# Performance work log

Hardware: AMD Instinct MI355X
Metric: run time of the kernel (lower is better)

Reference implementation:

```python
import jax, jax.numpy as jnp
import numpy as np

G, B, S, D = 4, 1, 1024, 2048   # num_gpus (chunks), batch, seq_local, model dim
H, DH = 32, 64                  # heads, dim_head; inner_dim = H*DH = D
EPS = 1e-6
NEG = -1e30                     # finite stand-in for -inf lse init (grad-safe)


def setup_inputs() -> dict:
    key = jax.random.key(0)
    ks = jax.random.split(key, 8)
    wsc = 1.0 / np.sqrt(D)  # keep pre-softmax logits in a sane range
    return {
        'x':  jax.random.normal(ks[0], (G, B, S, D), jnp.float32),
        'Wq': jax.random.normal(ks[1], (D, D), jnp.float32) * wsc,
        'bq': jnp.zeros((D,), jnp.float32),
        'Wk': jax.random.normal(ks[2], (D, D), jnp.float32) * wsc,
        'bk': jnp.zeros((D,), jnp.float32),
        'Wv': jax.random.normal(ks[3], (D, D), jnp.float32) * wsc,
        'bv': jnp.zeros((D,), jnp.float32),
        'qn_w': jnp.ones((D,), jnp.float32),
        'kn_w': jnp.ones((D,), jnp.float32),
        'Wo': jax.random.normal(ks[4], (D, D), jnp.float32) * wsc,
        'bo': jnp.zeros((D,), jnp.float32),
    }


def _rms_norm(t, w):
    return t * jax.lax.rsqrt(jnp.mean(t * t, axis=-1, keepdims=True) + EPS) * w


def reference(x, Wq, bq, Wk, bk, Wv, bv, qn_w, kn_w, Wo, bo):
    # x: [G, B, S, D] -- per-'GPU' sequence chunks
    q = _rms_norm(x @ Wq.T + bq, qn_w)
    k = _rms_norm(x @ Wk.T + bk, kn_w)
    v = x @ Wv.T + bv
    split = lambda t: t.reshape(G, B, S, H, DH).transpose(0, 1, 3, 2, 4)  # [G,B,H,S,DH]
    q, k, v = split(q), split(k), split(v)
    scale = 1.0 / np.sqrt(DH)

    out = jnp.zeros_like(q)
    lse = jnp.full((G, B, H, S, 1), NEG, q.dtype)
    kc, vc = k, v
    # Ring: each chunk attends to the visiting K/V chunk with online softmax.
    for _ in range(G):
        scores = jnp.einsum('gbhqd,gbhkd->gbhqk', q, kc) * scale
        m = scores.max(axis=-1, keepdims=True)
        e = jnp.exp(scores - m)
        ssum = e.sum(axis=-1, keepdims=True)
        chunk_lse = m + jnp.log(ssum)
        chunk_out = jnp.einsum('gbhqk,gbhkd->gbhqd', e / ssum, vc)
        new_lse = jnp.logaddexp(lse, chunk_lse)
        out = out * jnp.exp(lse - new_lse) + chunk_out * jnp.exp(chunk_lse - new_lse)
        lse = new_lse
        # rotate K/V around the ring: device i receives from device i-1
        kc = jnp.roll(kc, 1, axis=0)
        vc = jnp.roll(vc, 1, axis=0)

    o = out.transpose(0, 1, 3, 2, 4).reshape(G, B, S, H * DH)
    return o @ Wo.T + bo
```

## Files before the change

### kernel.cpp

```cpp
#include <hip/hip_runtime.h>

typedef __bf16 bf16x8 __attribute__((ext_vector_type(8)));
typedef float f32x4 __attribute__((ext_vector_type(4)));
typedef float f32x16 __attribute__((ext_vector_type(16)));
typedef unsigned short u16x8 __attribute__((ext_vector_type(8)));
typedef unsigned u32x2 __attribute__((ext_vector_type(2)));
typedef unsigned u32x4 __attribute__((ext_vector_type(4)));

__device__ __forceinline__ unsigned short f2bf(float f) {
  union { float f; unsigned u; } v; v.f = f;
  unsigned r = (v.u + 0x7fffu + ((v.u >> 16) & 1u)) >> 16;
  return (unsigned short)r;
}
__device__ __forceinline__ float bf2f(unsigned short s) {
  union { unsigned u; float f; } v; v.u = ((unsigned)s) << 16;
  return v.f;
}

#define GLD16(g, l)                                                        \
  __builtin_amdgcn_global_load_lds(                                        \
      (const __attribute__((address_space(1))) void*)(g),                  \
      (__attribute__((address_space(3))) void*)(l), 16, 0, 0)

__device__ __forceinline__ int swzc(int row, int colel) {
  return colel ^ ((((row & 7) ^ ((row >> 3) & 7)) & 7) << 3);
}

__device__ __forceinline__ u32x2 plswap(unsigned a, unsigned b) {
  return __builtin_amdgcn_permlane32_swap(a, b, false, false);
}
__device__ __forceinline__ float pair_max(float x) {
  u32x2 r = plswap(__float_as_uint(x), __float_as_uint(x));
  return fmaxf(__uint_as_float(r.x), __uint_as_float(r.y));
}
__device__ __forceinline__ float pair_sum(float x) {
  u32x2 r = plswap(__float_as_uint(x), __float_as_uint(x));
  return __uint_as_float(r.x) + __uint_as_float(r.y);
}
__device__ __forceinline__ unsigned cvtpk(float a, float b) {
  unsigned r;
  asm("v_cvt_pk_bf16_f32 %0, %1, %2" : "=v"(r) : "v"(a), "v"(b));
  return r;
}
__device__ __forceinline__ float F3(float a, float b, float c) {
  return fmaxf(fmaxf(a, b), c);
}

__global__ __launch_bounds__(256) void cast_bf16_kernel(
    const float* __restrict__ in, unsigned short* __restrict__ out, int n4) {
  int i = blockIdx.x * 256 + threadIdx.x;
  int stride = gridDim.x * 256;
  for (; i < n4; i += stride) {
    float4 f = reinterpret_cast<const float4*>(in)[i];
    ushort4 s;
    s.x = f2bf(f.x); s.y = f2bf(f.y); s.z = f2bf(f.z); s.w = f2bf(f.w);
    reinterpret_cast<ushort4*>(out)[i] = s;
  }
}

template <int F32OUT>
__global__ __launch_bounds__(256) void gemm_bt(
    const unsigned short* __restrict__ A, const unsigned short* __restrict__ B,
    const float* __restrict__ bias, void* __restrict__ Cp, int M, int N, int K) {
  __shared__ unsigned short As[128 * 64];
  __shared__ unsigned short Bs[128 * 64];
  const int tid = threadIdx.x;
  const int lane = tid & 63;
  const int wid = tid >> 6;
  const int wr = wid >> 1, wc = wid & 1;
  const int l15 = lane & 15, l4 = lane >> 4;
  const int row0 = blockIdx.y * 128, col0 = blockIdx.x * 128;

  f32x4 acc[4][4] = {};

  const int srow = lane >> 3;
  const int scol = (lane & 7) * 8;

  for (int kt = 0; kt < K; kt += 64) {
    __syncthreads();
#pragma unroll
    for (int i = 0; i < 4; ++i) {
      int c = wid * 4 + i;
      GLD16(A + (size_t)(row0 + c * 8 + srow) * K + kt + scol, &As[c * 512]);
      GLD16(B + (size_t)(col0 + c * 8 + srow) * K + kt + scol, &Bs[c * 512]);
    }
    __syncthreads();
#pragma unroll
    for (int ks = 0; ks < 2; ++ks) {
      const int ko = ks * 32 + l4 * 8;
      bf16x8 af[4], bfr[4];
#pragma unroll
      for (int mi = 0; mi < 4; ++mi)
        af[mi] = *(const bf16x8*)&As[(wr * 64 + mi * 16 + l15) * 64 + ko];
#pragma unroll
      for (int ni = 0; ni < 4; ++ni)
        bfr[ni] = *(const bf16x8*)&Bs[(wc * 64 + ni * 16 + l15) * 64 + ko];
#pragma unroll
      for (int mi = 0; mi < 4; ++mi)
#pragma unroll
        for (int ni = 0; ni < 4; ++ni)
          acc[mi][ni] = __builtin_amdgcn_mfma_f32_16x16x32_bf16(
              af[mi], bfr[ni], acc[mi][ni], 0, 0, 0);
    }
  }

#pragma unroll
  for (int mi = 0; mi < 4; ++mi)
#pragma unroll
    for (int ni = 0; ni < 4; ++ni)
#pragma unroll
      for (int r = 0; r < 4; ++r) {
        int row = row0 + wr * 64 + mi * 16 + l4 * 4 + r;
        int col = col0 + wc * 64 + ni * 16 + l15;
        float v = acc[mi][ni][r] + bias[col];
        if (F32OUT)
          ((float*)Cp)[(size_t)row * N + col] = v;
        else
          ((unsigned short*)Cp)[(size_t)row * N + col] = f2bf(v);
      }
}

__global__ __launch_bounds__(256) void rmsnorm_kernel(
    unsigned short* __restrict__ T, const float* __restrict__ w) {
  const int row = blockIdx.x;
  const int tid = threadIdx.x;
  unsigned short* p = T + (size_t)row * 2048;
  u16x8 v = *(const u16x8*)&p[tid * 8];
  float f[8];
  float ss = 0.f;
#pragma unroll
  for (int j = 0; j < 8; ++j) { f[j] = bf2f(v[j]); ss += f[j] * f[j]; }
#pragma unroll
  for (int m = 1; m < 64; m <<= 1) ss += __shfl_xor(ss, m, 64);
  __shared__ float red[4];
  const int wid = tid >> 6, lane = tid & 63;
  if (lane == 0) red[wid] = ss;
  __syncthreads();
  float tot = red[0] + red[1] + red[2] + red[3];
  float rs = rsqrtf(tot * (1.0f / 2048.0f) + 1e-6f);
  u16x8 o;
#pragma unroll
  for (int j = 0; j < 8; ++j) o[j] = f2bf(f[j] * rs * w[tid * 8 + j]);
  *(u16x8*)&p[tid * 8] = o;
}

__global__ __launch_bounds__(256, 4) void flash_attn(
    const unsigned short* __restrict__ Q, const unsigned short* __restrict__ K,
    const unsigned short* __restrict__ V, unsigned short* __restrict__ O) {
  __shared__ unsigned short Ks[2][64 * 64];
  __shared__ unsigned short Vs[2][64 * 64];
  const int bid = blockIdx.x;
  const int sw = (bid & 7) * 128 + (bid >> 3);
  const int h = sw >> 5;
  const int q0 = (sw & 31) * 128;
  const int tid = threadIdx.x, lane = tid & 63, wid = tid >> 6;
  const int l31 = lane & 31, hi = lane >> 5;

  const int kr0 = wid * 16 + (lane >> 3);
  const int kc0 = (lane & 7) * 8;
  const int vkey = (tid & 31) * 2;
  const int vd0 = (tid >> 5) * 8;

  const float QSCALE = 0.125f * 1.44269504f;
  bf16x8 qf[4];
  {
    const int qrow = q0 + wid * 32 + l31;
#pragma unroll
    for (int kt = 0; kt < 4; ++kt) {
      bf16x8 raw = *(const bf16x8*)&Q[(size_t)qrow * 2048 + h * 64 + kt * 16 + hi * 8];
#pragma unroll
      for (int j = 0; j < 8; ++j) qf[kt][j] = (__bf16)((float)raw[j] * QSCALE);
    }
  }

  float m_r = -1e30f, l_r = 0.f;
  f32x16 oa[2] = {};

  u16x8 kreg0, kreg1, vreg0, vreg1;
  auto loadKV = [&](int kt0) {
    kreg0 = *(const u16x8*)&K[(size_t)(kt0 + kr0) * 2048 + h * 64 + kc0];
    kreg1 = *(const u16x8*)&K[(size_t)(kt0 + kr0 + 8) * 2048 + h * 64 + kc0];
    vreg0 = *(const u16x8*)&V[(size_t)(kt0 + vkey) * 2048 + h * 64 + vd0];
    vreg1 = *(const u16x8*)&V[(size_t)(kt0 + vkey + 1) * 2048 + h * 64 + vd0];
  };
  auto writeKV = [&](int b) {
    *(u16x8*)&Ks[b][kr0 * 64 + swzc(kr0, kc0)] = kreg0;
    *(u16x8*)&Ks[b][(kr0 + 8) * 64 + swzc(kr0 + 8, kc0)] = kreg1;
#pragma unroll
    for (int d = 0; d < 8; ++d) {
      int row = vd0 + d;
      *(unsigned*)&Vs[b][row * 64 + swzc(row, vkey)] =
          (unsigned)vreg0[d] | ((unsigned)vreg1[d] << 16);
    }
  };

  loadKV(0);
  writeKV(0);
  __syncthreads();

  for (int t = 0; t < 64; ++t) {
    const int cur = t & 1;
    if (t < 63) loadKV((t + 1) * 64);

    f32x16 st[2];
    __builtin_amdgcn_s_setprio(1);
#pragma unroll
    for (int kb = 0; kb < 2; ++kb) {
      f32x16 a = {};
      const int row = kb * 32 + l31;
#pragma unroll
      for (int kt = 0; kt < 4; ++kt) {
        bf16x8 kf = *(const bf16x8*)&Ks[cur][row * 64 + swzc(row, kt * 16 + hi * 8)];
        a = __builtin_amdgcn_mfma_f32_32x32x16_bf16(kf, qf[kt], a, 0, 0, 0);
      }
      st[kb] = a;
    }
    __builtin_amdgcn_s_setprio(0);

    float t8[8];
#pragma unroll
    for (int j = 0; j < 8; ++j)
      t8[j] = fmaxf(F3(st[0][2 * j], st[0][2 * j + 1], st[1][2 * j]),
                    st[1][2 * j + 1]);
    float tmax = pair_max(F3(F3(t8[0], t8[1], t8[2]), F3(t8[3], t8[4], t8[5]),
                             fmaxf(t8[6], t8[7])));

    if (!__all(tmax <= m_r + 11.0f)) {
      float mn = fmaxf(m_r, tmax);
      float corr = __builtin_amdgcn_exp2f(m_r - mn);
      l_r *= corr;
#pragma unroll
      for (int dv = 0; dv < 2; ++dv)
#pragma unroll
        for (int r = 0; r < 16; ++r) oa[dv][r] *= corr;
      m_r = mn;
    }

    unsigned pk[16];
    float s0 = 0.f, s1 = 0.f, s2 = 0.f, s3 = 0.f;
#pragma unroll
    for (int kb = 0; kb < 2; ++kb)
#pragma unroll
      for (int j = 0; j < 8; ++j) {
        float pa = __builtin_amdgcn_exp2f(st[kb][2 * j] - m_r);
        float pb = __builtin_amdgcn_exp2f(st[kb][2 * j + 1] - m_r);
        if ((j & 3) == 0) s0 += pa + pb;
        else if ((j & 3) == 1) s1 += pa + pb;
        else if ((j & 3) == 2) s2 += pa + pb;
        else s3 += pa + pb;
        pk[kb * 8 + j] = cvtpk(pa, pb);
      }
    l_r += pair_sum(((s0 + s1) + (s2 + s3)));

    bf16x8 pfrag[4];
#pragma unroll
    for (int kt = 0; kt < 4; ++kt) {
      u32x2 sa = plswap(pk[4 * kt + 0], pk[4 * kt + 2]);
      u32x2 sb = plswap(pk[4 * kt + 1], pk[4 * kt + 3]);
      union { u32x4 u; bf16x8 b; } w;
      w.u.x = sa.x; w.u.y = sb.x; w.u.z = sa.y; w.u.w = sb.y;
      pfrag[kt] = w.b;
    }

    __builtin_amdgcn_s_setprio(1);
#pragma unroll
    for (int dv = 0; dv < 2; ++dv) {
      const int row = dv * 32 + l31;
#pragma unroll
      for (int kt = 0; kt < 4; ++kt) {
        bf16x8 vf = *(const bf16x8*)&Vs[cur][row * 64 + swzc(row, kt * 16 + hi * 8)];
        oa[dv] = __builtin_amdgcn_mfma_f32_32x32x16_bf16(vf, pfrag[kt], oa[dv], 0, 0, 0);
      }
    }
    __builtin_amdgcn_s_setprio(0);

    if (t < 63) {
      writeKV(cur ^ 1);
      __syncthreads();
    }
  }

  const float inv = 1.0f / l_r;
  const int qrow = q0 + wid * 32 + l31;
#pragma unroll
  for (int dv = 0; dv < 2; ++dv)
#pragma unroll
    for (int tq = 0; tq < 4; ++tq) {
      unsigned w0 = cvtpk(oa[dv][4 * tq + 0] * inv, oa[dv][4 * tq + 1] * inv);
      unsigned w1 = cvtpk(oa[dv][4 * tq + 2] * inv, oa[dv][4 * tq + 3] * inv);
      int dh = 32 * dv + 8 * tq + 4 * hi;
      u32x2 w2 = {w0, w1};
      *(u32x2*)&O[(size_t)qrow * 2048 + h * 64 + dh] = w2;
    }
}

extern "C" void kernel_launch(void* const* d_in, const int* in_sizes, int n_in,
                              void* d_out, int out_size, void* d_ws, size_t ws_size,
                              hipStream_t stream) {
  const float* x  = (const float*)d_in[0];
  const float* Wq = (const float*)d_in[1];
  const float* bq = (const float*)d_in[2];
  const float* Wk = (const float*)d_in[3];
  const float* bk = (const float*)d_in[4];
  const float* Wv = (const float*)d_in[5];
  const float* bv = (const float*)d_in[6];
  const float* qn = (const float*)d_in[7];
  const float* kn = (const float*)d_in[8];
  const float* Wo = (const float*)d_in[9];
  const float* bo = (const float*)d_in[10];

  char* w = (char*)d_ws;
  unsigned short* Xbf = (unsigned short*)(w);
  unsigned short* Wqb = (unsigned short*)(w + 16777216);
  unsigned short* Wkb = (unsigned short*)(w + 25165824);
  unsigned short* Wvb = (unsigned short*)(w + 33554432);
  unsigned short* Wob = (unsigned short*)(w + 41943040);
  unsigned short* Qb  = (unsigned short*)(w + 50331648);
  unsigned short* Kb  = (unsigned short*)(w + 67108864);
  unsigned short* Vb  = (unsigned short*)(w + 83886080);
  unsigned short* Ob  = Xbf;

  const int M = 4096, N = 2048, Kd = 2048;

  cast_bf16_kernel<<<1024, 256, 0, stream>>>(x,  Xbf, 8388608 / 4);
  cast_bf16_kernel<<<512, 256, 0, stream>>>(Wq, Wqb, 4194304 / 4);
  cast_bf16_kernel<<<512, 256, 0, stream>>>(Wk, Wkb, 4194304 / 4);
  cast_bf16_kernel<<<512, 256, 0, stream>>>(Wv, Wvb, 4194304 / 4);
  cast_bf16_kernel<<<512, 256, 0, stream>>>(Wo, Wob, 4194304 / 4);

  dim3 gg(N / 128, M / 128);
  gemm_bt<0><<<gg, 256, 0, stream>>>(Xbf, Wqb, bq, Qb, M, N, Kd);
  gemm_bt<0><<<gg, 256, 0, stream>>>(Xbf, Wkb, bk, Kb, M, N, Kd);
  gemm_bt<0><<<gg, 256, 0, stream>>>(Xbf, Wvb, bv, Vb, M, N, Kd);

  rmsnorm_kernel<<<4096, 256, 0, stream>>>(Qb, qn);
  rmsnorm_kernel<<<4096, 256, 0, stream>>>(Kb, kn);

  flash_attn<<<1024, 256, 0, stream>>>(Qb, Kb, Vb, Ob);

  gemm_bt<1><<<gg, 256, 0, stream>>>(Ob, Wob, bo, (float*)d_out, M, N, Kd);
}
```

Baseline: 425.4 us.

## Fuse QKV GEMMs, weight casts, rmsnorms; swizzle blocks; MFMA row-sum in attention

Merges the four weight casts into one launch, the three QKV projections into one GEMM grid with per-column-block weight selection, and the two rmsnorms into one launch. Adds grouped block-index swizzling to both GEMMs for L2 reuse. In flash attention it precomputes swizzled LDS offsets and replaces the per-thread softmax row-sum and cross-lane reduction with an extra MFMA against a ones vector. The goal is fewer launches and less VALU work in the softmax loop, at the cost of extra MFMA work and bf16-rounded P in the denominator.

```diff
diff --git a/kernel.cpp b/kernel.cpp
--- a/kernel.cpp
+++ b/kernel.cpp
@@ -32,10 +32,6 @@
 __device__ __forceinline__ float pair_max(float x) {
   u32x2 r = plswap(__float_as_uint(x), __float_as_uint(x));
   return fmaxf(__uint_as_float(r.x), __uint_as_float(r.y));
-}
-__device__ __forceinline__ float pair_sum(float x) {
-  u32x2 r = plswap(__float_as_uint(x), __float_as_uint(x));
-  return __uint_as_float(r.x) + __uint_as_float(r.y);
 }
 __device__ __forceinline__ unsigned cvtpk(float a, float b) {
   unsigned r;
@@ -58,10 +54,47 @@
   }
 }
 
-template <int F32OUT>
-__global__ __launch_bounds__(256) void gemm_bt(
-    const unsigned short* __restrict__ A, const unsigned short* __restrict__ B,
-    const float* __restrict__ bias, void* __restrict__ Cp, int M, int N, int K) {
+__global__ __launch_bounds__(256) void cast_w4_kernel(
+    const float* __restrict__ w0, const float* __restrict__ w1,
+    const float* __restrict__ w2, const float* __restrict__ w3,
+    unsigned short* __restrict__ o0, unsigned short* __restrict__ o1,
+    unsigned short* __restrict__ o2, unsigned short* __restrict__ o3) {
+  int i = blockIdx.x * 256 + threadIdx.x;
+  int stride = gridDim.x * 256;
+  for (; i < 4194304; i += stride) {
+    int sel = i >> 20;
+    const float* src = sel == 0 ? w0 : sel == 1 ? w1 : sel == 2 ? w2 : w3;
+    unsigned short* dst = sel == 0 ? o0 : sel == 1 ? o1 : sel == 2 ? o2 : o3;
+    int j = i & 1048575;
+    float4 f = reinterpret_cast<const float4*>(src)[j];
+    ushort4 s;
+    s.x = f2bf(f.x); s.y = f2bf(f.y); s.z = f2bf(f.z); s.w = f2bf(f.w);
+    reinterpret_cast<ushort4*>(dst)[j] = s;
+  }
+}
+
+__global__ __launch_bounds__(256) void gemm_qkv(
+    const unsigned short* __restrict__ A,
+    const unsigned short* __restrict__ W0, const unsigned short* __restrict__ W1,
+    const unsigned short* __restrict__ W2,
+    const float* __restrict__ b0, const float* __restrict__ b1,
+    const float* __restrict__ b2,
+    unsigned short* __restrict__ C0, unsigned short* __restrict__ C1,
+    unsigned short* __restrict__ C2) {
+  const int K = 2048, N = 2048;
+  const int lin = blockIdx.x + blockIdx.y * gridDim.x;
+  const int cpx = (gridDim.x * gridDim.y) >> 3;
+  const int swz = (lin & 7) * cpx + (lin >> 3);
+  const int bx = swz % gridDim.x, by = swz / gridDim.x;
+
+  const int gcol = bx * 128;
+  const int sel = gcol >> 11;
+  const unsigned short* B = sel == 0 ? W0 : sel == 1 ? W1 : W2;
+  const float* bias = sel == 0 ? b0 : sel == 1 ? b1 : b2;
+  unsigned short* Cp = sel == 0 ? C0 : sel == 1 ? C1 : C2;
+  const int col0 = gcol & 2047;
+  const int row0 = by * 128;
+
   __shared__ unsigned short As[128 * 64];
   __shared__ unsigned short Bs[128 * 64];
   const int tid = threadIdx.x;
@@ -69,7 +102,6 @@
   const int wid = tid >> 6;
   const int wr = wid >> 1, wc = wid & 1;
   const int l15 = lane & 15, l4 = lane >> 4;
-  const int row0 = blockIdx.y * 128, col0 = blockIdx.x * 128;
 
   f32x4 acc[4][4] = {};
 
@@ -113,18 +145,81 @@
         int row = row0 + wr * 64 + mi * 16 + l4 * 4 + r;
         int col = col0 + wc * 64 + ni * 16 + l15;
         float v = acc[mi][ni][r] + bias[col];
-        if (F32OUT)
-          ((float*)Cp)[(size_t)row * N + col] = v;
-        else
-          ((unsigned short*)Cp)[(size_t)row * N + col] = f2bf(v);
+        Cp[(size_t)row * N + col] = f2bf(v);
       }
 }
 
-__global__ __launch_bounds__(256) void rmsnorm_kernel(
-    unsigned short* __restrict__ T, const float* __restrict__ w) {
+__global__ __launch_bounds__(256) void gemm_bt_f32(
+    const unsigned short* __restrict__ A, const unsigned short* __restrict__ B,
+    const float* __restrict__ bias, float* __restrict__ Cp, int M, int N, int K) {
+  const int lin = blockIdx.x + blockIdx.y * gridDim.x;
+  const int cpx = (gridDim.x * gridDim.y) >> 3;
+  const int swz = (lin & 7) * cpx + (lin >> 3);
+  const int bx = swz % gridDim.x, by = swz / gridDim.x;
+
+  __shared__ unsigned short As[128 * 64];
+  __shared__ unsigned short Bs[128 * 64];
+  const int tid = threadIdx.x;
+  const int lane = tid & 63;
+  const int wid = tid >> 6;
+  const int wr = wid >> 1, wc = wid & 1;
+  const int l15 = lane & 15, l4 = lane >> 4;
+  const int row0 = by * 128, col0 = bx * 128;
+
+  f32x4 acc[4][4] = {};
+
+  const int srow = lane >> 3;
+  const int scol = (lane & 7) * 8;
+
+  for (int kt = 0; kt < K; kt += 64) {
+    __syncthreads();
+#pragma unroll
+    for (int i = 0; i < 4; ++i) {
+      int c = wid * 4 + i;
+      GLD16(A + (size_t)(row0 + c * 8 + srow) * K + kt + scol, &As[c * 512]);
+      GLD16(B + (size_t)(col0 + c * 8 + srow) * K + kt + scol, &Bs[c * 512]);
+    }
+    __syncthreads();
+#pragma unroll
+    for (int ks = 0; ks < 2; ++ks) {
+      const int ko = ks * 32 + l4 * 8;
+      bf16x8 af[4], bfr[4];
+#pragma unroll
+      for (int mi = 0; mi < 4; ++mi)
+        af[mi] = *(const bf16x8*)&As[(wr * 64 + mi * 16 + l15) * 64 + ko];
+#pragma unroll
+      for (int ni = 0; ni < 4; ++ni)
+        bfr[ni] = *(const bf16x8*)&Bs[(wc * 64 + ni * 16 + l15) * 64 + ko];
+#pragma unroll
+      for (int mi = 0; mi < 4; ++mi)
+#pragma unroll
+        for (int ni = 0; ni < 4; ++ni)
+          acc[mi][ni] = __builtin_amdgcn_mfma_f32_16x16x32_bf16(
+              af[mi], bfr[ni], acc[mi][ni], 0, 0, 0);
+    }
+  }
+
+#pragma unroll
+  for (int mi = 0; mi < 4; ++mi)
+#pragma unroll
+    for (int ni = 0; ni < 4; ++ni)
+#pragma unroll
+      for (int r = 0; r < 4; ++r) {
+        int row = row0 + wr * 64 + mi * 16 + l4 * 4 + r;
+        int col = col0 + wc * 64 + ni * 16 + l15;
+        Cp[(size_t)row * N + col] = acc[mi][ni][r] + bias[col];
+      }
+}
+
+__global__ __launch_bounds__(256) void rmsnorm2_kernel(
+    unsigned short* __restrict__ Qb, unsigned short* __restrict__ Kb,
+    const float* __restrict__ qw, const float* __restrict__ kw) {
   const int row = blockIdx.x;
+  unsigned short* p;
+  const float* w;
+  if (row < 4096) { p = Qb + (size_t)row * 2048; w = qw; }
+  else            { p = Kb + (size_t)(row - 4096) * 2048; w = kw; }
   const int tid = threadIdx.x;
-  unsigned short* p = T + (size_t)row * 2048;
   u16x8 v = *(const u16x8*)&p[tid * 8];
   float f[8];
   float ss = 0.f;
@@ -173,8 +268,23 @@
     }
   }
 
-  float m_r = -1e30f, l_r = 0.f;
+  int off[2][4];
+#pragma unroll
+  for (int kb = 0; kb < 2; ++kb) {
+    const int row = kb * 32 + l31;
+    const int sel = (((row & 7) ^ ((row >> 3) & 7)) & 7) << 3;
+#pragma unroll
+    for (int kt = 0; kt < 4; ++kt)
+      off[kb][kt] = row * 64 + ((kt * 16 + hi * 8) ^ sel);
+  }
+
+  bf16x8 onesf;
+#pragma unroll
+  for (int j = 0; j < 8; ++j) onesf[j] = (__bf16)1.0f;
+
+  float m_r = -1e30f;
   f32x16 oa[2] = {};
+  f32x16 lacc = {};
 
   u16x8 kreg0, kreg1, vreg0, vreg1;
   auto loadKV = [&](int kt0) {
@@ -202,15 +312,17 @@
     const int cur = t & 1;
     if (t < 63) loadKV((t + 1) * 64);
 
+    const unsigned short* Kc = Ks[cur];
+    const unsigned short* Vc = Vs[cur];
+
     f32x16 st[2];
     __builtin_amdgcn_s_setprio(1);
 #pragma unroll
     for (int kb = 0; kb < 2; ++kb) {
       f32x16 a = {};
-      const int row = kb * 32 + l31;
 #pragma unroll
       for (int kt = 0; kt < 4; ++kt) {
-        bf16x8 kf = *(const bf16x8*)&Ks[cur][row * 64 + swzc(row, kt * 16 + hi * 8)];
+        bf16x8 kf = *(const bf16x8*)&Kc[off[kb][kt]];
         a = __builtin_amdgcn_mfma_f32_32x32x16_bf16(kf, qf[kt], a, 0, 0, 0);
       }
       st[kb] = a;
@@ -228,7 +340,7 @@
     if (!__all(tmax <= m_r + 11.0f)) {
       float mn = fmaxf(m_r, tmax);
       float corr = __builtin_amdgcn_exp2f(m_r - mn);
-      l_r *= corr;
+      lacc[0] *= corr;
 #pragma unroll
       for (int dv = 0; dv < 2; ++dv)
 #pragma unroll
@@ -237,20 +349,14 @@
     }
 
     unsigned pk[16];
-    float s0 = 0.f, s1 = 0.f, s2 = 0.f, s3 = 0.f;
 #pragma unroll
     for (int kb = 0; kb < 2; ++kb)
 #pragma unroll
       for (int j = 0; j < 8; ++j) {
         float pa = __builtin_amdgcn_exp2f(st[kb][2 * j] - m_r);
         float pb = __builtin_amdgcn_exp2f(st[kb][2 * j + 1] - m_r);
-        if ((j & 3) == 0) s0 += pa + pb;
-        else if ((j & 3) == 1) s1 += pa + pb;
-        else if ((j & 3) == 2) s2 += pa + pb;
-        else s3 += pa + pb;
         pk[kb * 8 + j] = cvtpk(pa, pb);
       }
-    l_r += pair_sum(((s0 + s1) + (s2 + s3)));
 
     bf16x8 pfrag[4];
 #pragma unroll
@@ -264,11 +370,13 @@
 
     __builtin_amdgcn_s_setprio(1);
 #pragma unroll
+    for (int kt = 0; kt < 4; ++kt)
+      lacc = __builtin_amdgcn_mfma_f32_32x32x16_bf16(onesf, pfrag[kt], lacc, 0, 0, 0);
+#pragma unroll
     for (int dv = 0; dv < 2; ++dv) {
-      const int row = dv * 32 + l31;
 #pragma unroll
       for (int kt = 0; kt < 4; ++kt) {
-        bf16x8 vf = *(const bf16x8*)&Vs[cur][row * 64 + swzc(row, kt * 16 + hi * 8)];
+        bf16x8 vf = *(const bf16x8*)&Vc[off[dv][kt]];
         oa[dv] = __builtin_amdgcn_mfma_f32_32x32x16_bf16(vf, pfrag[kt], oa[dv], 0, 0, 0);
       }
     }
@@ -280,7 +388,7 @@
     }
   }
 
-  const float inv = 1.0f / l_r;
+  const float inv = 1.0f / lacc[0];
   const int qrow = q0 + wid * 32 + l31;
 #pragma unroll
   for (int dv = 0; dv < 2; ++dv)
@@ -320,23 +428,16 @@
   unsigned short* Vb  = (unsigned short*)(w + 83886080);
   unsigned short* Ob  = Xbf;
 
-  const int M = 4096, N = 2048, Kd = 2048;
-
-  cast_bf16_kernel<<<1024, 256, 0, stream>>>(x,  Xbf, 8388608 / 4);
-  cast_bf16_kernel<<<512, 256, 0, stream>>>(Wq, Wqb, 4194304 / 4);
-  cast_bf16_kernel<<<512, 256, 0, stream>>>(Wk, Wkb, 4194304 / 4);
-  cast_bf16_kernel<<<512, 256, 0, stream>>>(Wv, Wvb, 4194304 / 4);
-  cast_bf16_kernel<<<512, 256, 0, stream>>>(Wo, Wob, 4194304 / 4);
-
-  dim3 gg(N / 128, M / 128);
-  gemm_bt<0><<<gg, 256, 0, stream>>>(Xbf, Wqb, bq, Qb, M, N, Kd);
-  gemm_bt<0><<<gg, 256, 0, stream>>>(Xbf, Wkb, bk, Kb, M, N, Kd);
-  gemm_bt<0><<<gg, 256, 0, stream>>>(Xbf, Wvb, bv, Vb, M, N, Kd);
-
-  rmsnorm_kernel<<<4096, 256, 0, stream>>>(Qb, qn);
-  rmsnorm_kernel<<<4096, 256, 0, stream>>>(Kb, kn);
+  cast_bf16_kernel<<<1024, 256, 0, stream>>>(x, Xbf, 8388608 / 4);
+  cast_w4_kernel<<<2048, 256, 0, stream>>>(Wq, Wk, Wv, Wo, Wqb, Wkb, Wvb, Wob);
+
+  gemm_qkv<<<dim3(48, 32), 256, 0, stream>>>(Xbf, Wqb, Wkb, Wvb, bq, bk, bv,
+                                             Qb, Kb, Vb);
+
+  rmsnorm2_kernel<<<8192, 256, 0, stream>>>(Qb, Kb, qn, kn);
 
   flash_attn<<<1024, 256, 0, stream>>>(Qb, Kb, Vb, Ob);
 
-  gemm_bt<1><<<gg, 256, 0, stream>>>(Ob, Wob, bo, (float*)d_out, M, N, Kd);
-}
+  gemm_bt_f32<<<dim3(16, 32), 256, 0, stream>>>(Ob, Wob, bo, (float*)d_out,
+                                                4096, 2048, 2048);
+}
```

Result: slower. 442.7 us (+4.1%).

## Pipeline GEMM with multi-stage LDS buffering and merge QKV/cast/rmsnorm launches

Applied to the files above, without the earlier changes.

Replaces the single-buffered GEMM with an 8-phase software-pipelined kernel. It uses double-buffered LDS tiles split by k-half, swizzled LDS layout, explicit vmcnt waits, and a grouped block-index swizzle for L2 locality. The Q/K/V projections become one fused launch over a 48-wide grid, and the four weight casts and two rmsnorms are each merged into a single launch. The attention kernel precomputes its swizzled LDS offsets once instead of recomputing them every iteration. The manual waitcnt scheduling is fragile and uses 64KB of dynamic LDS per block.

```diff
diff --git a/kernel.cpp b/kernel.cpp
--- a/kernel.cpp
+++ b/kernel.cpp
@@ -58,73 +58,178 @@
   }
 }
 
+__global__ __launch_bounds__(256) void cast_w4_kernel(
+    const float* __restrict__ w0, const float* __restrict__ w1,
+    const float* __restrict__ w2, const float* __restrict__ w3,
+    unsigned short* __restrict__ o0, unsigned short* __restrict__ o1,
+    unsigned short* __restrict__ o2, unsigned short* __restrict__ o3) {
+  int i = blockIdx.x * 256 + threadIdx.x;
+  int stride = gridDim.x * 256;
+  for (; i < 4194304; i += stride) {
+    int sel = i >> 20;
+    const float* src = sel == 0 ? w0 : sel == 1 ? w1 : sel == 2 ? w2 : w3;
+    unsigned short* dst = sel == 0 ? o0 : sel == 1 ? o1 : sel == 2 ? o2 : o3;
+    int j = i & 1048575;
+    float4 f = reinterpret_cast<const float4*>(src)[j];
+    ushort4 s;
+    s.x = f2bf(f.x); s.y = f2bf(f.y); s.z = f2bf(f.z); s.w = f2bf(f.w);
+    reinterpret_cast<ushort4*>(dst)[j] = s;
+  }
+}
+
+
+#define STG_A(STEP, KS, BUF)                                                   \
+  GLD16(Ag + (size_t)(row0 + st_row0) * 2048 + (STEP) * 64 + (KS) * 32 +       \
+            st_col0,                                                           \
+        &ls[((BUF) * 2 + (KS)) * 4096 + (wid * 2) * 512]);                     \
+  GLD16(Ag + (size_t)(row0 + st_row1) * 2048 + (STEP) * 64 + (KS) * 32 +       \
+            st_col1,                                                           \
+        &ls[((BUF) * 2 + (KS)) * 4096 + (wid * 2 + 1) * 512]);
+
+#define STG_B(STEP, KS, BUF)                                                   \
+  GLD16(Bg + (size_t)(col0 + st_row0) * 2048 + (STEP) * 64 + (KS) * 32 +       \
+            st_col0,                                                           \
+        &ls[16384 + ((BUF) * 2 + (KS)) * 4096 + (wid * 2) * 512]);             \
+  GLD16(Bg + (size_t)(col0 + st_row1) * 2048 + (STEP) * 64 + (KS) * 32 +       \
+            st_col1,                                                           \
+        &ls[16384 + ((BUF) * 2 + (KS)) * 4096 + (wid * 2 + 1) * 512]);
+
+#define VM8 asm volatile("s_waitcnt vmcnt(8)" ::: "memory");
+#define VM4 asm volatile("s_waitcnt vmcnt(4)" ::: "memory");
+#define VM0 asm volatile("s_waitcnt vmcnt(0)" ::: "memory");
+
+#define PHASE(BUF, KS, MQ, RB, STG, VMW)                                       \
+  {                                                                            \
+    af0 = *(const bf16x8*)&ls[((BUF) * 2 + (KS)) * 4096 + offA[(MQ) * 2 + 0]]; \
+    af1 = *(const bf16x8*)&ls[((BUF) * 2 + (KS)) * 4096 + offA[(MQ) * 2 + 1]]; \
+    if (RB) {                                                                  \
+      bfr[0] = *(const bf16x8*)&ls[16384 + ((BUF) * 2 + (KS)) * 4096 + offB[0]]; \
+      bfr[1] = *(const bf16x8*)&ls[16384 + ((BUF) * 2 + (KS)) * 4096 + offB[1]]; \
+      bfr[2] = *(const bf16x8*)&ls[16384 + ((BUF) * 2 + (KS)) * 4096 + offB[2]]; \
+      bfr[3] = *(const bf16x8*)&ls[16384 + ((BUF) * 2 + (KS)) * 4096 + offB[3]]; \
+    }                                                                          \
+    STG;                                                                       \
+    __builtin_amdgcn_s_barrier();                                              \
+    __builtin_amdgcn_s_setprio(1);                                             \
+    acc[(MQ) * 2 + 0][0] = __builtin_amdgcn_mfma_f32_16x16x32_bf16(            \
+        af0, bfr[0], acc[(MQ) * 2 + 0][0], 0, 0, 0);                           \
+    acc[(MQ) * 2 + 0][1] = __builtin_amdgcn_mfma_f32_16x16x32_bf16(            \
+        af0, bfr[1], acc[(MQ) * 2 + 0][1], 0, 0, 0);                           \
+    acc[(MQ) * 2 + 0][2] = __builtin_amdgcn_mfma_f32_16x16x32_bf16(            \
+        af0, bfr[2], acc[(MQ) * 2 + 0][2], 0, 0, 0);                           \
+    acc[(MQ) * 2 + 0][3] = __builtin_amdgcn_mfma_f32_16x16x32_bf16(            \
+        af0, bfr[3], acc[(MQ) * 2 + 0][3], 0, 0, 0);                           \
+    acc[(MQ) * 2 + 1][0] = __builtin_amdgcn_mfma_f32_16x16x32_bf16(            \
+        af1, bfr[0], acc[(MQ) * 2 + 1][0], 0, 0, 0);                           \
+    acc[(MQ) * 2 + 1][1] = __builtin_amdgcn_mfma_f32_16x16x32_bf16(            \
+        af1, bfr[1], acc[(MQ) * 2 + 1][1], 0, 0, 0);                           \
+    acc[(MQ) * 2 + 1][2] = __builtin_amdgcn_mfma_f32_16x16x32_bf16(            \
+        af1, bfr[2], acc[(MQ) * 2 + 1][2], 0, 0, 0);                           \
+    acc[(MQ) * 2 + 1][3] = __builtin_amdgcn_mfma_f32_16x16x32_bf16(            \
+        af1, bfr[3], acc[(MQ) * 2 + 1][3], 0, 0, 0);                           \
+    __builtin_amdgcn_s_setprio(0);                                             \
+    VMW;                                                                       \
+    __builtin_amdgcn_s_barrier();                                              \
+  }
+
 template <int F32OUT>
-__global__ __launch_bounds__(256) void gemm_bt(
-    const unsigned short* __restrict__ A, const unsigned short* __restrict__ B,
-    const float* __restrict__ bias, void* __restrict__ Cp, int M, int N, int K) {
-  __shared__ unsigned short As[128 * 64];
-  __shared__ unsigned short Bs[128 * 64];
+__global__ __launch_bounds__(256, 2) void gemm8p(
+    const unsigned short* __restrict__ Ag,
+    const unsigned short* __restrict__ W0, const unsigned short* __restrict__ W1,
+    const unsigned short* __restrict__ W2,
+    const float* __restrict__ b0, const float* __restrict__ b1,
+    const float* __restrict__ b2,
+    void* __restrict__ C0, void* __restrict__ C1, void* __restrict__ C2) {
+  extern __shared__ __align__(16) unsigned short ls[];
+
+  const int lin = blockIdx.y * gridDim.x + blockIdx.x;
+  const int cpx = (gridDim.x * gridDim.y) >> 3;
+  const int swz = (lin & 7) * cpx + (lin >> 3);
+  const int bx = swz % gridDim.x, by = swz / gridDim.x;
+
+  const int gcol = bx * 128;
+  const int sel = gcol >> 11;
+  const unsigned short* Bg = sel == 0 ? W0 : sel == 1 ? W1 : W2;
+  const float* bias = sel == 0 ? b0 : sel == 1 ? b1 : b2;
+  void* Cp = sel == 0 ? C0 : sel == 1 ? C1 : C2;
+  const int col0 = gcol & 2047;
+  const int row0 = by * 128;
+
+  const int tid = threadIdx.x, lane = tid & 63, wid = tid >> 6;
+  const int l15 = lane & 15, l4 = lane >> 4;
+  const int wm = wid >> 1, wn = wid & 1;
+
+  const int ci0 = wid * 2, ci1 = wid * 2 + 1;
+  const int st_row0 = ci0 * 16 + (lane >> 2);
+  const int st_row1 = ci1 * 16 + (lane >> 2);
+  const int sl2a = ((lane >> 2) & 3) ^ ((lane >> 4) & 3);
+  const int st_col0 = (((lane & 3) ^ (sl2a ^ (ci0 & 3))) * 8);
+  const int st_col1 = (((lane & 3) ^ (sl2a ^ (ci1 & 3))) * 8);
+
+  const int lsel = (l15 & 3) ^ ((l15 >> 2) & 3);
+  int offA[4], offB[4];
+#pragma unroll
+  for (int f = 0; f < 4; ++f)
+    offA[f] = (wm * 64 + f * 16 + l15) * 32 + ((l4 ^ lsel ^ (f & 3)) & 3) * 8;
+#pragma unroll
+  for (int ni = 0; ni < 4; ++ni)
+    offB[ni] =
+        (wn * 64 + ni * 16 + l15) * 32 + ((l4 ^ lsel ^ ((wn * 4 + ni) & 3)) & 3) * 8;
+
+  f32x4 acc[4][4] = {};
+  bf16x8 af0, af1, bfr[4];
+
+  STG_A(0, 0, 0); STG_B(0, 0, 0);
+  STG_A(0, 1, 0); STG_B(0, 1, 0);
+  STG_A(1, 0, 1); STG_B(1, 0, 1);
+  VM8;
+  __builtin_amdgcn_s_barrier();
+
+  for (int it = 0; it < 15; ++it) {
+    const int sE = 2 * it, sO = sE + 1;
+    PHASE(0, 0, 0, 1, STG_A(sO, 1, 1), );
+    PHASE(0, 0, 1, 0, STG_B(sO, 1, 1), VM8);
+    PHASE(0, 1, 0, 1, STG_A(sE + 2, 0, 0), );
+    PHASE(0, 1, 1, 0, STG_B(sE + 2, 0, 0), VM8);
+    PHASE(1, 0, 0, 1, STG_A(sE + 2, 1, 0), );
+    PHASE(1, 0, 1, 0, STG_B(sE + 2, 1, 0), VM8);
+    PHASE(1, 1, 0, 1, STG_A(sO + 2, 0, 1), );
+    PHASE(1, 1, 1, 0, STG_B(sO + 2, 0, 1), VM8);
+  }
+  PHASE(0, 0, 0, 1, STG_A(31, 1, 1), );
+  PHASE(0, 0, 1, 0, STG_B(31, 1, 1), VM8);
+  PHASE(0, 1, 0, 1, , );
+  PHASE(0, 1, 1, 0, , VM4);
+  PHASE(1, 0, 0, 1, , );
+  PHASE(1, 0, 1, 0, , VM0);
+  PHASE(1, 1, 0, 1, , );
+  PHASE(1, 1, 1, 0, , );
+
+#pragma unroll
+  for (int f = 0; f < 4; ++f)
+#pragma unroll
+    for (int ni = 0; ni < 4; ++ni)
+#pragma unroll
+      for (int r = 0; r < 4; ++r) {
+        int row = row0 + wm * 64 + f * 16 + l4 * 4 + r;
+        int col = col0 + wn * 64 + ni * 16 + l15;
+        float v = acc[f][ni][r] + bias[col];
+        if (F32OUT)
+          ((float*)Cp)[(size_t)row * 2048 + col] = v;
+        else
+          ((unsigned short*)Cp)[(size_t)row * 2048 + col] = f2bf(v);
+      }
+}
+
+__global__ __launch_bounds__(256) void rmsnorm2_kernel(
+    unsigned short* __restrict__ Qb, unsigned short* __restrict__ Kb,
+    const float* __restrict__ qw, const float* __restrict__ kw) {
+  const int row = blockIdx.x;
+  unsigned short* p;
+  const float* w;
+  if (row < 4096) { p = Qb + (size_t)row * 2048; w = qw; }
+  else            { p = Kb + (size_t)(row - 4096) * 2048; w = kw; }
   const int tid = threadIdx.x;
-  const int lane = tid & 63;
-  const int wid = tid >> 6;
-  const int wr = wid >> 1, wc = wid & 1;
-  const int l15 = lane & 15, l4 = lane >> 4;
-  const int row0 = blockIdx.y * 128, col0 = blockIdx.x * 128;
-
-  f32x4 acc[4][4] = {};
-
-  const int srow = lane >> 3;
-  const int scol = (lane & 7) * 8;
-
-  for (int kt = 0; kt < K; kt += 64) {
-    __syncthreads();
-#pragma unroll
-    for (int i = 0; i < 4; ++i) {
-      int c = wid * 4 + i;
-      GLD16(A + (size_t)(row0 + c * 8 + srow) * K + kt + scol, &As[c * 512]);
-      GLD16(B + (size_t)(col0 + c * 8 + srow) * K + kt + scol, &Bs[c * 512]);
-    }
-    __syncthreads();
-#pragma unroll
-    for (int ks = 0; ks < 2; ++ks) {
-      const int ko = ks * 32 + l4 * 8;
-      bf16x8 af[4], bfr[4];
-#pragma unroll
-      for (int mi = 0; mi < 4; ++mi)
-        af[mi] = *(const bf16x8*)&As[(wr * 64 + mi * 16 + l15) * 64 + ko];
-#pragma unroll
-      for (int ni = 0; ni < 4; ++ni)
-        bfr[ni] = *(const bf16x8*)&Bs[(wc * 64 + ni * 16 + l15) * 64 + ko];
-#pragma unroll
-      for (int mi = 0; mi < 4; ++mi)
-#pragma unroll
-        for (int ni = 0; ni < 4; ++ni)
-          acc[mi][ni] = __builtin_amdgcn_mfma_f32_16x16x32_bf16(
-              af[mi], bfr[ni], acc[mi][ni], 0, 0, 0);
-    }
-  }
-
-#pragma unroll
-  for (int mi = 0; mi < 4; ++mi)
-#pragma unroll
-    for (int ni = 0; ni < 4; ++ni)
-#pragma unroll
-      for (int r = 0; r < 4; ++r) {
-        int row = row0 + wr * 64 + mi * 16 + l4 * 4 + r;
-        int col = col0 + wc * 64 + ni * 16 + l15;
-        float v = acc[mi][ni][r] + bias[col];
-        if (F32OUT)
-          ((float*)Cp)[(size_t)row * N + col] = v;
-        else
-          ((unsigned short*)Cp)[(size_t)row * N + col] = f2bf(v);
-      }
-}
-
-__global__ __launch_bounds__(256) void rmsnorm_kernel(
-    unsigned short* __restrict__ T, const float* __restrict__ w) {
-  const int row = blockIdx.x;
-  const int tid = threadIdx.x;
-  unsigned short* p = T + (size_t)row * 2048;
   u16x8 v = *(const u16x8*)&p[tid * 8];
   float f[8];
   float ss = 0.f;
@@ -173,6 +278,16 @@
     }
   }
 
+  int off[2][4];
+#pragma unroll
+  for (int kb = 0; kb < 2; ++kb) {
+    const int row = kb * 32 + l31;
+    const int sl = (((row & 7) ^ ((row >> 3) & 7)) & 7) << 3;
+#pragma unroll
+    for (int kt = 0; kt < 4; ++kt)
+      off[kb][kt] = row * 64 + ((kt * 16 + hi * 8) ^ sl);
+  }
+
   float m_r = -1e30f, l_r = 0.f;
   f32x16 oa[2] = {};
 
@@ -202,15 +317,17 @@
     const int cur = t & 1;
     if (t < 63) loadKV((t + 1) * 64);
 
+    const unsigned short* Kc = Ks[cur];
+    const unsigned short* Vc = Vs[cur];
+
     f32x16 st[2];
     __builtin_amdgcn_s_setprio(1);
 #pragma unroll
     for (int kb = 0; kb < 2; ++kb) {
       f32x16 a = {};
-      const int row = kb * 32 + l31;
 #pragma unroll
       for (int kt = 0; kt < 4; ++kt) {
-        bf16x8 kf = *(const bf16x8*)&Ks[cur][row * 64 + swzc(row, kt * 16 + hi * 8)];
+        bf16x8 kf = *(const bf16x8*)&Kc[off[kb][kt]];
         a = __builtin_amdgcn_mfma_f32_32x32x16_bf16(kf, qf[kt], a, 0, 0, 0);
       }
       st[kb] = a;
@@ -265,10 +382,9 @@
     __builtin_amdgcn_s_setprio(1);
 #pragma unroll
     for (int dv = 0; dv < 2; ++dv) {
-      const int row = dv * 32 + l31;
 #pragma unroll
       for (int kt = 0; kt < 4; ++kt) {
-        bf16x8 vf = *(const bf16x8*)&Vs[cur][row * 64 + swzc(row, kt * 16 + hi * 8)];
+        bf16x8 vf = *(const bf16x8*)&Vc[off[dv][kt]];
         oa[dv] = __builtin_amdgcn_mfma_f32_32x32x16_bf16(vf, pfrag[kt], oa[dv], 0, 0, 0);
       }
     }
@@ -320,23 +436,16 @@
   unsigned short* Vb  = (unsigned short*)(w + 83886080);
   unsigned short* Ob  = Xbf;
 
-  const int M = 4096, N = 2048, Kd = 2048;
-
-  cast_bf16_kernel<<<1024, 256, 0, stream>>>(x,  Xbf, 8388608 / 4);
-  cast_bf16_kernel<<<512, 256, 0, stream>>>(Wq, Wqb, 4194304 / 4);
-  cast_bf16_kernel<<<512, 256, 0, stream>>>(Wk, Wkb, 4194304 / 4);
-  cast_bf16_kernel<<<512, 256, 0, stream>>>(Wv, Wvb, 4194304 / 4);
-  cast_bf16_kernel<<<512, 256, 0, stream>>>(Wo, Wob, 4194304 / 4);
-
-  dim3 gg(N / 128, M / 128);
-  gemm_bt<0><<<gg, 256, 0, stream>>>(Xbf, Wqb, bq, Qb, M, N, Kd);
-  gemm_bt<0><<<gg, 256, 0, stream>>>(Xbf, Wkb, bk, Kb, M, N, Kd);
-  gemm_bt<0><<<gg, 256, 0, stream>>>(Xbf, Wvb, bv, Vb, M, N, Kd);
-
-  rmsnorm_kernel<<<4096, 256, 0, stream>>>(Qb, qn);
-  rmsnorm_kernel<<<4096, 256, 0, stream>>>(Kb, kn);
+  cast_bf16_kernel<<<1024, 256, 0, stream>>>(x, Xbf, 8388608 / 4);
+  cast_w4_kernel<<<2048, 256, 0, stream>>>(Wq, Wk, Wv, Wo, Wqb, Wkb, Wvb, Wob);
+
+  gemm8p<0><<<dim3(48, 32), 256, 65536, stream>>>(
+      Xbf, Wqb, Wkb, Wvb, bq, bk, bv, Qb, Kb, Vb);
+
+  rmsnorm2_kernel<<<8192, 256, 0, stream>>>(Qb, Kb, qn, kn);
 
   flash_attn<<<1024, 256, 0, stream>>>(Qb, Kb, Vb, Ob);
 
-  gemm_bt<1><<<gg, 256, 0, stream>>>(Ob, Wob, bo, (float*)d_out, M, N, Kd);
-}
+  gemm8p<1><<<dim3(16, 32), 256, 65536, stream>>>(
+      Ob, Wob, Wob, Wob, bo, bo, bo, d_out, d_out, d_out);
+}
```

Result: faster. 395.4 us (-7.1%).
